# Performance work log

Hardware: AMD Instinct MI355X
Metric: run time of the kernel (lower is better)

## Reference

```python
import jax, jax.numpy as jnp
import numpy as np
import math

B, S, D, H, FF = 8, 1024, 1024, 16, 4096
DH = D // H
EPS = 1e-5


def _layernorm(x, g, b):
    mu = jnp.mean(x, axis=-1, keepdims=True)
    var = jnp.mean((x - mu) ** 2, axis=-1, keepdims=True)
    return (x - mu) * jax.lax.rsqrt(var + EPS) * g + b


def _gelu_tanh(x):
    c = math.sqrt(2.0 / math.pi)
    return 0.5 * x * (1.0 + jnp.tanh(c * (x + 0.044715 * x ** 3)))


def setup_inputs() -> dict:
    key = jax.random.key(0)
    ks = jax.random.split(key, 8)
    s = lambda d: 1.0 / math.sqrt(d)
    return {
        "x": jax.random.normal(ks[0], (B, S, D), jnp.float32),
        "ln1_g": jnp.ones((D,), jnp.float32),
        "ln1_b": jnp.zeros((D,), jnp.float32),
        "w_qkv": jax.random.normal(ks[1], (3 * D, D), jnp.float32) * s(D),
        "b_qkv": jax.random.normal(ks[2], (3 * D,), jnp.float32) * 0.02,
        "w_o": jax.random.normal(ks[3], (D, D), jnp.float32) * s(D),
        "b_o": jax.random.normal(ks[4], (D,), jnp.float32) * 0.02,
        "ln2_g": jnp.ones((D,), jnp.float32),
        "ln2_b": jnp.zeros((D,), jnp.float32),
        "w1": jax.random.normal(ks[5], (FF, D), jnp.float32) * s(D),
        "b1": jax.random.normal(ks[6], (FF,), jnp.float32) * 0.02,
        "w2": jax.random.normal(ks[7], (D, FF), jnp.float32) * s(FF),
        "b2": jnp.zeros((D,), jnp.float32),
    }


def reference(x, ln1_g, ln1_b, w_qkv, b_qkv, w_o, b_o, ln2_g, ln2_b, w1, b1, w2, b2):
    # --- pre-LN causal self-attention ---
    h = _layernorm(x, ln1_g, ln1_b)
    qkv = h @ w_qkv.T + b_qkv                      # [B,S,3D]
    q, k, v = jnp.split(qkv, 3, axis=-1)
    q = q.reshape(B, S, H, DH)
    k = k.reshape(B, S, H, DH)
    v = v.reshape(B, S, H, DH)
    scores = jnp.einsum("bqhd,bkhd->bhqk", q, k) / math.sqrt(DH)
    causal = jnp.triu(jnp.ones((S, S), jnp.bool_), 1)  # True above diagonal
    scores = jnp.where(causal, -jnp.inf, scores)
    attn = jax.nn.softmax(scores, axis=-1)
    o = jnp.einsum("bhqk,bkhd->bqhd", attn, v).reshape(B, S, D)
    x = x + (o @ w_o.T + b_o)
    # --- FFN ---
    h = _layernorm(x, ln2_g, ln2_b)
    h = _gelu_tanh(h @ w1.T + b1) @ w2.T + b2
    return x + h
```

## Files before the change

kernel.cpp:

```cpp
#include <hip/hip_runtime.h>
#include <math.h>


typedef __bf16 bf16_t;
typedef __bf16 bf16x4 __attribute__((ext_vector_type(4)));
typedef __bf16 bf16x8 __attribute__((ext_vector_type(8)));
typedef float f32x4 __attribute__((ext_vector_type(4)));

__device__ __forceinline__ void async16(const void* g, void* l) {
    __builtin_amdgcn_global_load_lds(
        (const __attribute__((address_space(1))) void*)g,
        (__attribute__((address_space(3))) void*)l,
        16, 0, 0);
}

__global__ __launch_bounds__(256) void f2b4(const float* __restrict__ in,
                                            bf16_t* __restrict__ out) {
    const int i = (blockIdx.x * 256 + threadIdx.x) * 4;
    const float4 v = *(const float4*)(in + i);
    bf16x4 o;
    o[0] = (bf16_t)v.x; o[1] = (bf16_t)v.y; o[2] = (bf16_t)v.z; o[3] = (bf16_t)v.w;
    *(bf16x4*)(out + i) = o;
}

__global__ __launch_bounds__(256) void ln_bf16(const float* __restrict__ x,
                                               const float* __restrict__ g,
                                               const float* __restrict__ bb,
                                               bf16_t* __restrict__ out) {
    const int tid = threadIdx.x;
    const int row = blockIdx.x;
    const float4 xv = *(const float4*)(x + row * 1024 + tid * 4);
    float s1 = xv.x + xv.y + xv.z + xv.w;
    float s2 = xv.x * xv.x + xv.y * xv.y + xv.z * xv.z + xv.w * xv.w;
#pragma unroll
    for (int m = 32; m >= 1; m >>= 1) {
        s1 += __shfl_xor(s1, m);
        s2 += __shfl_xor(s2, m);
    }
    __shared__ float r1[4], r2[4];
    const int wid = tid >> 6, lane = tid & 63;
    if (lane == 0) { r1[wid] = s1; r2[wid] = s2; }
    __syncthreads();
    s1 = r1[0] + r1[1] + r1[2] + r1[3];
    s2 = r2[0] + r2[1] + r2[2] + r2[3];
    const float mu = s1 * (1.0f / 1024.0f);
    const float var = s2 * (1.0f / 1024.0f) - mu * mu;
    const float rs = rsqrtf(var + 1e-5f);
    const float4 gv = *(const float4*)(g + tid * 4);
    const float4 bv = *(const float4*)(bb + tid * 4);
    bf16x4 o;
    o[0] = (bf16_t)((xv.x - mu) * rs * gv.x + bv.x);
    o[1] = (bf16_t)((xv.y - mu) * rs * gv.y + bv.y);
    o[2] = (bf16_t)((xv.z - mu) * rs * gv.z + bv.z);
    o[3] = (bf16_t)((xv.w - mu) * rs * gv.w + bv.w);
    *(bf16x4*)(out + row * 1024 + tid * 4) = o;
}

template <int MODE>
__global__ __launch_bounds__(256, 2) void gemm_bt(
    const bf16_t* __restrict__ A, const bf16_t* __restrict__ W,
    const float* __restrict__ bias, const float* __restrict__ resid,
    bf16_t* __restrict__ outb, float* __restrict__ outf, int N, int K) {
    __shared__ bf16_t As[128 * 64];
    __shared__ bf16_t Bs[128 * 64];
    const int tid = threadIdx.x;
    const int w = tid >> 6;
    const int lane = tid & 63;
    const int l15 = lane & 15;
    const int quad = lane >> 4;

    const int nbn = N >> 7;
    const int per = 8 * nbn;
    const int lid = blockIdx.x;
    const int bm = (lid / per) * 8 + (lid % per) % 8;
    const int bn = (lid % per) / 8;
    const int m0 = bm * 128;
    const int n0 = bn * 128;
    const int wm = (w & 1) * 64;
    const int wn = (w >> 1) * 64;

    int rr[4], so[4];
#pragma unroll
    for (int q = 0; q < 4; q++) {
        const int c = q * 256 + w * 64 + lane;
        rr[q] = c >> 3;
        so[q] = ((c & 7) ^ (rr[q] & 7)) * 8;
    }
    const bf16_t* pA[4];
    const bf16_t* pB[4];
#pragma unroll
    for (int q = 0; q < 4; q++) {
        pA[q] = A + (size_t)(m0 + rr[q]) * K + so[q];
        pB[q] = W + (size_t)(n0 + rr[q]) * K + so[q];
    }

    f32x4 acc[4][4] = {};

    for (int k0 = 0; k0 < K; k0 += 64) {
#pragma unroll
        for (int q = 0; q < 4; q++) {
            async16(pA[q], As + q * 2048 + w * 512);
            async16(pB[q], Bs + q * 2048 + w * 512);
            pA[q] += 64; pB[q] += 64;
        }
        __syncthreads();

        bf16x8 af[4][2], bfr[4][2];
#pragma unroll
        for (int i = 0; i < 4; i++) {
            const int r = wm + i * 16 + l15;
#pragma unroll
            for (int f = 0; f < 2; f++) {
                const int slot = (f * 4 + quad) ^ (r & 7);
                af[i][f] = *(const bf16x8*)(As + r * 64 + slot * 8);
            }
        }
#pragma unroll
        for (int j = 0; j < 4; j++) {
            const int r = wn + j * 16 + l15;
#pragma unroll
            for (int f = 0; f < 2; f++) {
                const int slot = (f * 4 + quad) ^ (r & 7);
                bfr[j][f] = *(const bf16x8*)(Bs + r * 64 + slot * 8);
            }
        }
#pragma unroll
        for (int i = 0; i < 4; i++)
#pragma unroll
            for (int j = 0; j < 4; j++)
#pragma unroll
                for (int f = 0; f < 2; f++)
                    acc[i][j] = __builtin_amdgcn_mfma_f32_16x16x32_bf16(
                        af[i][f], bfr[j][f], acc[i][j], 0, 0, 0);
        __syncthreads();
    }

    const int er = quad * 4;
#pragma unroll
    for (int i = 0; i < 4; i++) {
#pragma unroll
        for (int j = 0; j < 4; j++) {
#pragma unroll
            for (int r = 0; r < 4; r++) {
                const int row = m0 + wm + i * 16 + er + r;
                const int col = n0 + wn + j * 16 + l15;
                float v = acc[i][j][r] + bias[col];
                if (MODE == 1) {
                    const float u = 0.7978845608028654f * (v + 0.044715f * v * v * v);
                    v = 0.5f * v * (1.0f + tanhf(u));
                }
                const size_t idx = (size_t)row * N + col;
                if (MODE == 2) {
                    outf[idx] = v + resid[idx];
                } else {
                    outb[idx] = (bf16_t)v;
                }
            }
        }
    }
}

__global__ __launch_bounds__(256) void vtrans(const bf16_t* __restrict__ qkv,
                                              bf16_t* __restrict__ vt) {
    const int wid = threadIdx.x >> 6;
    const int lane = threadIdx.x & 63;
    const int bh = blockIdx.y;
    const int b = bh >> 4, h = bh & 15;
    const int so = blockIdx.x * 4 + wid;
    const bf16_t* src = qkv + (size_t)(b * 1024 + so * 8) * 3072 + 2048 + h * 64 + lane;
    bf16x8 v;
#pragma unroll
    for (int i = 0; i < 8; i++) v[i] = src[i * 3072];
    *(bf16x8*)(vt + ((size_t)bh * 64 + lane) * 1024 + so * 8) = v;
}

__global__ __launch_bounds__(256) void attn_mfma(const bf16_t* __restrict__ qkv,
                                                 const bf16_t* __restrict__ vt,
                                                 bf16_t* __restrict__ o) {
    __shared__ bf16_t Ks[4096];
    __shared__ bf16_t Vs[4096];
    __shared__ bf16_t Ps[4][16][72];
    const int tid = threadIdx.x;
    const int w = tid >> 6;
    const int lane = tid & 63;
    const int l15 = lane & 15;
    const int quad = lane >> 4;
    const int qb = blockIdx.x;
    const int bh = blockIdx.y;
    const int b = bh >> 4, h = bh & 15;

    const int qrow = b * 1024 + qb * 64 + w * 16;
    const int qmaxw = qb * 64 + w * 16 + 15;

    bf16x8 qf[2];
#pragma unroll
    for (int f = 0; f < 2; f++) {
        bf16x8 t = *(const bf16x8*)(qkv + (size_t)(qrow + l15) * 3072 + h * 64 + f * 32 + quad * 8);
#pragma unroll
        for (int e = 0; e < 8; e++) t[e] = (bf16_t)((float)t[e] * 0.125f);
        qf[f] = t;
    }

    f32x4 Ot[4] = {};
    float mrow = -3.0e38f, lrow = 0.0f;

    const int c0 = w * 64 + lane;
    const int c1 = 256 + c0;
    const int r0 = c0 >> 3, g0 = (((c0 & 7) ^ (r0 & 7))) * 8;
    const int r1 = c1 >> 3, g1 = (((c1 & 7) ^ (r1 & 7))) * 8;

    const bf16_t* kbase = qkv + (size_t)(b * 1024) * 3072 + 1024 + h * 64;
    const bf16_t* vbase = vt + (size_t)bh * 64 * 1024;

    for (int kt = 0; kt <= qb; kt++) {
        async16(kbase + (size_t)(kt * 64 + r0) * 3072 + g0, Ks + w * 512);
        async16(kbase + (size_t)(kt * 64 + r1) * 3072 + g1, Ks + 2048 + w * 512);
        async16(vbase + (size_t)r0 * 1024 + kt * 64 + g0, Vs + w * 512);
        async16(vbase + (size_t)r1 * 1024 + kt * 64 + g1, Vs + 2048 + w * 512);
        __syncthreads();

        f32x4 sf[4];
#pragma unroll
        for (int kb = 0; kb < 4; kb++) {
            if (kt * 64 + kb * 16 > qmaxw) {
                sf[kb] = (f32x4){-3.0e38f, -3.0e38f, -3.0e38f, -3.0e38f};
                continue;
            }
            const int r = kb * 16 + l15;
            f32x4 acc = {};
#pragma unroll
            for (int f = 0; f < 2; f++) {
                const int seg = (f * 4 + quad) ^ (r & 7);
                const bf16x8 kf = *(const bf16x8*)(Ks + r * 64 + seg * 8);
                acc = __builtin_amdgcn_mfma_f32_16x16x32_bf16(kf, qf[f], acc, 0, 0, 0);
            }
            if (kt == qb && kb == w) {
#pragma unroll
                for (int rr2 = 0; rr2 < 4; rr2++)
                    if (quad * 4 + rr2 > l15) acc[rr2] = -3.0e38f;
            }
            sf[kb] = acc;
        }

        float tmax = -3.0e38f;
#pragma unroll
        for (int kb = 0; kb < 4; kb++)
#pragma unroll
            for (int rr2 = 0; rr2 < 4; rr2++) tmax = fmaxf(tmax, sf[kb][rr2]);
        tmax = fmaxf(tmax, __shfl_xor(tmax, 16));
        tmax = fmaxf(tmax, __shfl_xor(tmax, 32));
        const float mnew = fmaxf(mrow, tmax);
        const float alpha = __expf(mrow - mnew);
        float psum = 0.0f;
#pragma unroll
        for (int kb = 0; kb < 4; kb++) {
            bf16x4 pk;
#pragma unroll
            for (int rr2 = 0; rr2 < 4; rr2++) {
                const float p = __expf(sf[kb][rr2] - mnew);
                psum += p;
                pk[rr2] = (bf16_t)p;
            }
            *(bf16x4*)(&Ps[w][l15][kb * 16 + quad * 4]) = pk;
        }
        psum += __shfl_xor(psum, 16);
        psum += __shfl_xor(psum, 32);
        lrow = lrow * alpha + psum;
        mrow = mnew;
#pragma unroll
        for (int db = 0; db < 4; db++)
#pragma unroll
            for (int rr2 = 0; rr2 < 4; rr2++) Ot[db][rr2] *= alpha;

#pragma unroll
        for (int ks = 0; ks < 2; ks++) {
            if (kt * 64 + ks * 32 > qmaxw) break;
            const bf16x8 pf = *(const bf16x8*)(&Ps[w][l15][ks * 32 + quad * 8]);
#pragma unroll
            for (int db = 0; db < 4; db++) {
                const int d = db * 16 + l15;
                const int seg = (ks * 4 + quad) ^ (d & 7);
                const bf16x8 vf = *(const bf16x8*)(Vs + d * 64 + seg * 8);
                Ot[db] = __builtin_amdgcn_mfma_f32_16x16x32_bf16(vf, pf, Ot[db], 0, 0, 0);
            }
        }
        __syncthreads();
    }

    const float rl = 1.0f / lrow;
#pragma unroll
    for (int db = 0; db < 4; db++) {
        bf16x4 ov;
#pragma unroll
        for (int rr2 = 0; rr2 < 4; rr2++) ov[rr2] = (bf16_t)(Ot[db][rr2] * rl);
        *(bf16x4*)(o + (size_t)(qrow + l15) * 1024 + h * 64 + db * 16 + quad * 4) = ov;
    }
}

extern "C" void kernel_launch(void* const* d_in, const int* in_sizes, int n_in,
                              void* d_out, int out_size, void* d_ws, size_t ws_size,
                              hipStream_t stream) {
    const float* x     = (const float*)d_in[0];
    const float* ln1g  = (const float*)d_in[1];
    const float* ln1b  = (const float*)d_in[2];
    const float* w_qkv = (const float*)d_in[3];
    const float* b_qkv = (const float*)d_in[4];
    const float* w_o   = (const float*)d_in[5];
    const float* b_o   = (const float*)d_in[6];
    const float* ln2g  = (const float*)d_in[7];
    const float* ln2b  = (const float*)d_in[8];
    const float* w1    = (const float*)d_in[9];
    const float* b1    = (const float*)d_in[10];
    const float* w2    = (const float*)d_in[11];
    const float* b2    = (const float*)d_in[12];
    float* out = (float*)d_out;

    char* w = (char*)d_ws;
    bf16_t* wbqkv = (bf16_t*)(w + 0);
    bf16_t* wbo   = (bf16_t*)(w + 6291456);
    bf16_t* wb1   = (bf16_t*)(w + 8388608);
    bf16_t* wb2   = (bf16_t*)(w + 16777216);
    bf16_t* h     = (bf16_t*)(w + 25165824);
    bf16_t* qkv   = (bf16_t*)(w + 41943040);
    bf16_t* ob    = (bf16_t*)(w + 92274688);
    float*  x1    = (float*)(w + 109051904);
    bf16_t* f     = (bf16_t*)(w + 142606336);
    bf16_t* vtb   = (bf16_t*)(w + 142606336);

    f2b4<<<3072, 256, 0, stream>>>(w_qkv, wbqkv);
    f2b4<<<1024, 256, 0, stream>>>(w_o, wbo);
    f2b4<<<4096, 256, 0, stream>>>(w1, wb1);
    f2b4<<<4096, 256, 0, stream>>>(w2, wb2);

    ln_bf16<<<8192, 256, 0, stream>>>(x, ln1g, ln1b, h);
    gemm_bt<0><<<64 * 24, 256, 0, stream>>>(h, wbqkv, b_qkv, nullptr, qkv, nullptr, 3072, 1024);
    vtrans<<<dim3(32, 128), 256, 0, stream>>>(qkv, vtb);
    attn_mfma<<<dim3(16, 128), 256, 0, stream>>>(qkv, vtb, ob);
    gemm_bt<2><<<64 * 8, 256, 0, stream>>>(ob, wbo, b_o, x, nullptr, x1, 1024, 1024);
    ln_bf16<<<8192, 256, 0, stream>>>(x1, ln2g, ln2b, h);
    gemm_bt<1><<<64 * 32, 256, 0, stream>>>(h, wb1, b1, nullptr, f, nullptr, 4096, 1024);
    gemm_bt<2><<<64 * 8, 256, 0, stream>>>(f, wb2, b2, x1, nullptr, out, 1024, 4096);
}
```

Baseline: 503.6 us.

## Use 32x32 MFMA in GEMM, fuse V transpose into QKV epilogue, merge weight casts

Measured after the change: 506.2 us. Within noise of the previous version (+0.5%).

```diff
diff --git a/kernel.cpp b/kernel.cpp
--- a/kernel.cpp
+++ b/kernel.cpp
@@ -6,6 +6,7 @@
 typedef __bf16 bf16x4 __attribute__((ext_vector_type(4)));
 typedef __bf16 bf16x8 __attribute__((ext_vector_type(8)));
 typedef float f32x4 __attribute__((ext_vector_type(4)));
+typedef float f32x16 __attribute__((ext_vector_type(16)));
 
 __device__ __forceinline__ void async16(const void* g, void* l) {
     __builtin_amdgcn_global_load_lds(
@@ -14,13 +15,24 @@
         16, 0, 0);
 }
 
-__global__ __launch_bounds__(256) void f2b4(const float* __restrict__ in,
-                                            bf16_t* __restrict__ out) {
-    const int i = (blockIdx.x * 256 + threadIdx.x) * 4;
-    const float4 v = *(const float4*)(in + i);
+__global__ __launch_bounds__(256) void f2b_all(
+    const float* __restrict__ s0, const float* __restrict__ s1,
+    const float* __restrict__ s2, const float* __restrict__ s3,
+    bf16_t* __restrict__ d0, bf16_t* __restrict__ d1,
+    bf16_t* __restrict__ d2, bf16_t* __restrict__ d3) {
+    const int g = blockIdx.x * 256 + threadIdx.x;
+    const float* s;
+    bf16_t* d;
+    int off;
+    if (g < 786432)       { s = s0; d = d0; off = g; }
+    else if (g < 1048576) { s = s1; d = d1; off = g - 786432; }
+    else if (g < 2097152) { s = s2; d = d2; off = g - 1048576; }
+    else                  { s = s3; d = d3; off = g - 2097152; }
+    const int i = off * 4;
+    const float4 v = *(const float4*)(s + i);
     bf16x4 o;
     o[0] = (bf16_t)v.x; o[1] = (bf16_t)v.y; o[2] = (bf16_t)v.z; o[3] = (bf16_t)v.w;
-    *(bf16x4*)(out + i) = o;
+    *(bf16x4*)(d + i) = o;
 }
 
 __global__ __launch_bounds__(256) void ln_bf16(const float* __restrict__ x,
@@ -60,14 +72,15 @@
 __global__ __launch_bounds__(256, 2) void gemm_bt(
     const bf16_t* __restrict__ A, const bf16_t* __restrict__ W,
     const float* __restrict__ bias, const float* __restrict__ resid,
-    bf16_t* __restrict__ outb, float* __restrict__ outf, int N, int K) {
+    bf16_t* __restrict__ outb, float* __restrict__ outf,
+    bf16_t* __restrict__ vt, int N, int K) {
     __shared__ bf16_t As[128 * 64];
     __shared__ bf16_t Bs[128 * 64];
     const int tid = threadIdx.x;
     const int w = tid >> 6;
     const int lane = tid & 63;
-    const int l15 = lane & 15;
-    const int quad = lane >> 4;
+    const int l31 = lane & 31;
+    const int kh = lane >> 5;
 
     const int nbn = N >> 7;
     const int per = 8 * nbn;
@@ -94,7 +107,7 @@
         pB[q] = W + (size_t)(n0 + rr[q]) * K + so[q];
     }
 
-    f32x4 acc[4][4] = {};
+    f32x16 acc[2][2] = {};
 
     for (int k0 = 0; k0 < K; k0 += 64) {
 #pragma unroll
@@ -105,73 +118,76 @@
         }
         __syncthreads();
 
-        bf16x8 af[4][2], bfr[4][2];
-#pragma unroll
-        for (int i = 0; i < 4; i++) {
-            const int r = wm + i * 16 + l15;
-#pragma unroll
-            for (int f = 0; f < 2; f++) {
-                const int slot = (f * 4 + quad) ^ (r & 7);
-                af[i][f] = *(const bf16x8*)(As + r * 64 + slot * 8);
-            }
-        }
-#pragma unroll
-        for (int j = 0; j < 4; j++) {
-            const int r = wn + j * 16 + l15;
-#pragma unroll
-            for (int f = 0; f < 2; f++) {
-                const int slot = (f * 4 + quad) ^ (r & 7);
-                bfr[j][f] = *(const bf16x8*)(Bs + r * 64 + slot * 8);
-            }
-        }
-#pragma unroll
-        for (int i = 0; i < 4; i++)
-#pragma unroll
-            for (int j = 0; j < 4; j++)
-#pragma unroll
-                for (int f = 0; f < 2; f++)
-                    acc[i][j] = __builtin_amdgcn_mfma_f32_16x16x32_bf16(
-                        af[i][f], bfr[j][f], acc[i][j], 0, 0, 0);
+        bf16x8 af[2][4], bff[2][4];
+#pragma unroll
+        for (int mb = 0; mb < 2; mb++) {
+            const int r = wm + mb * 32 + l31;
+#pragma unroll
+            for (int ks = 0; ks < 4; ks++) {
+                const int slot = (ks * 2 + kh) ^ (r & 7);
+                af[mb][ks] = *(const bf16x8*)(As + r * 64 + slot * 8);
+            }
+        }
+#pragma unroll
+        for (int nb = 0; nb < 2; nb++) {
+            const int r = wn + nb * 32 + l31;
+#pragma unroll
+            for (int ks = 0; ks < 4; ks++) {
+                const int slot = (ks * 2 + kh) ^ (r & 7);
+                bff[nb][ks] = *(const bf16x8*)(Bs + r * 64 + slot * 8);
+            }
+        }
+#pragma unroll
+        for (int ks = 0; ks < 4; ks++)
+#pragma unroll
+            for (int mb = 0; mb < 2; mb++)
+#pragma unroll
+                for (int nb = 0; nb < 2; nb++)
+                    acc[mb][nb] = __builtin_amdgcn_mfma_f32_32x32x16_bf16(
+                        af[mb][ks], bff[nb][ks], acc[mb][nb], 0, 0, 0);
         __syncthreads();
     }
 
-    const int er = quad * 4;
-#pragma unroll
-    for (int i = 0; i < 4; i++) {
-#pragma unroll
-        for (int j = 0; j < 4; j++) {
-#pragma unroll
-            for (int r = 0; r < 4; r++) {
-                const int row = m0 + wm + i * 16 + er + r;
-                const int col = n0 + wn + j * 16 + l15;
-                float v = acc[i][j][r] + bias[col];
-                if (MODE == 1) {
-                    const float u = 0.7978845608028654f * (v + 0.044715f * v * v * v);
-                    v = 0.5f * v * (1.0f + tanhf(u));
+#pragma unroll
+    for (int mb = 0; mb < 2; mb++) {
+#pragma unroll
+        for (int nb = 0; nb < 2; nb++) {
+            const int col = n0 + wn + nb * 32 + l31;
+            const float bcol = bias[col];
+#pragma unroll
+            for (int g = 0; g < 4; g++) {
+                const int row0 = m0 + wm + mb * 32 + 8 * g + 4 * kh;
+                float v4[4];
+#pragma unroll
+                for (int q = 0; q < 4; q++) {
+                    float v = acc[mb][nb][4 * g + q] + bcol;
+                    if (MODE == 1) {
+                        const float u2 = -1.5957691216057308f * (v + 0.044715f * v * v * v);
+                        v = v * __builtin_amdgcn_rcpf(1.0f + __expf(u2));
+                    }
+                    v4[q] = v;
                 }
-                const size_t idx = (size_t)row * N + col;
                 if (MODE == 2) {
-                    outf[idx] = v + resid[idx];
+#pragma unroll
+                    for (int q = 0; q < 4; q++) {
+                        const size_t idx = (size_t)(row0 + q) * N + col;
+                        outf[idx] = v4[q] + resid[idx];
+                    }
+                } else if (MODE == 3 && col >= 2048) {
+                    const int bh = (row0 >> 10) * 16 + ((col - 2048) >> 6);
+                    const int d = (col - 2048) & 63;
+                    bf16x4 pk;
+#pragma unroll
+                    for (int q = 0; q < 4; q++) pk[q] = (bf16_t)v4[q];
+                    *(bf16x4*)(vt + (size_t)bh * 65536 + d * 1024 + (row0 & 1023)) = pk;
                 } else {
-                    outb[idx] = (bf16_t)v;
+#pragma unroll
+                    for (int q = 0; q < 4; q++)
+                        outb[(size_t)(row0 + q) * N + col] = (bf16_t)v4[q];
                 }
             }
         }
     }
-}
-
-__global__ __launch_bounds__(256) void vtrans(const bf16_t* __restrict__ qkv,
-                                              bf16_t* __restrict__ vt) {
-    const int wid = threadIdx.x >> 6;
-    const int lane = threadIdx.x & 63;
-    const int bh = blockIdx.y;
-    const int b = bh >> 4, h = bh & 15;
-    const int so = blockIdx.x * 4 + wid;
-    const bf16_t* src = qkv + (size_t)(b * 1024 + so * 8) * 3072 + 2048 + h * 64 + lane;
-    bf16x8 v;
-#pragma unroll
-    for (int i = 0; i < 8; i++) v[i] = src[i * 3072];
-    *(bf16x8*)(vt + ((size_t)bh * 64 + lane) * 1024 + so * 8) = v;
 }
 
 __global__ __launch_bounds__(256) void attn_mfma(const bf16_t* __restrict__ qkv,
@@ -327,17 +343,13 @@
     bf16_t* f     = (bf16_t*)(w + 142606336);
     bf16_t* vtb   = (bf16_t*)(w + 142606336);
 
-    f2b4<<<3072, 256, 0, stream>>>(w_qkv, wbqkv);
-    f2b4<<<1024, 256, 0, stream>>>(w_o, wbo);
-    f2b4<<<4096, 256, 0, stream>>>(w1, wb1);
-    f2b4<<<4096, 256, 0, stream>>>(w2, wb2);
+    f2b_all<<<12288, 256, 0, stream>>>(w_qkv, w_o, w1, w2, wbqkv, wbo, wb1, wb2);
 
     ln_bf16<<<8192, 256, 0, stream>>>(x, ln1g, ln1b, h);
-    gemm_bt<0><<<64 * 24, 256, 0, stream>>>(h, wbqkv, b_qkv, nullptr, qkv, nullptr, 3072, 1024);
-    vtrans<<<dim3(32, 128), 256, 0, stream>>>(qkv, vtb);
+    gemm_bt<3><<<64 * 24, 256, 0, stream>>>(h, wbqkv, b_qkv, nullptr, qkv, nullptr, vtb, 3072, 1024);
     attn_mfma<<<dim3(16, 128), 256, 0, stream>>>(qkv, vtb, ob);
-    gemm_bt<2><<<64 * 8, 256, 0, stream>>>(ob, wbo, b_o, x, nullptr, x1, 1024, 1024);
+    gemm_bt<2><<<64 * 8, 256, 0, stream>>>(ob, wbo, b_o, x, nullptr, x1, nullptr, 1024, 1024);
     ln_bf16<<<8192, 256, 0, stream>>>(x1, ln2g, ln2b, h);
-    gemm_bt<1><<<64 * 32, 256, 0, stream>>>(h, wb1, b1, nullptr, f, nullptr, 4096, 1024);
-    gemm_bt<2><<<64 * 8, 256, 0, stream>>>(f, wb2, b2, x1, nullptr, out, 1024, 4096);
-}
+    gemm_bt<1><<<64 * 32, 256, 0, stream>>>(h, wb1, b1, nullptr, f, nullptr, nullptr, 4096, 1024);
+    gemm_bt<2><<<64 * 8, 256, 0, stream>>>(f, wb2, b2, x1, nullptr, out, nullptr, 1024, 4096);
+}
```
